# Performance work log

Hardware: AMD Instinct MI355X
Metric: run time of the kernel (lower is better)

Reference implementation:

```python
import jax, jax.numpy as jnp
from jax import lax
import numpy as np

IN_C = 256
PREV_IN_C = 256
OUT_C = 128
ATTN = IN_C // 8  # attn_size == attn_out == 32


def setup_inputs() -> dict:
    key = jax.random.key(0)
    ks = jax.random.split(key, 12)
    B, W, H = 4, 64, 64
    s = 0.02
    return {
        "source_enc_f": jax.random.normal(ks[0], (B, IN_C, W, H), jnp.float32),
        "target_enc_f": jax.random.normal(ks[1], (B, IN_C, W, H), jnp.float32),
        "prev_inp": jax.random.normal(ks[2], (B, PREV_IN_C, W // 2, H // 2), jnp.float32),
        "key_w": s * jax.random.normal(ks[3], (ATTN, IN_C), jnp.float32),
        "key_b": jnp.zeros((ATTN,), jnp.float32),
        "query_w": s * jax.random.normal(ks[4], (ATTN, IN_C), jnp.float32),
        "query_b": jnp.zeros((ATTN,), jnp.float32),
        "lin_w": s * jax.random.normal(ks[5], (ATTN, 2 * ATTN), jnp.float32),  # k_q_linear: cat([key, query])
        "lin_b": jnp.zeros((ATTN,), jnp.float32),
        "attn_w": s * jax.random.normal(ks[6], (IN_C, ATTN + IN_C), jnp.float32),
        "attn_b": jnp.zeros((IN_C,), jnp.float32),
        "gamma": jnp.array(0.1, jnp.float32),  # torch inits 0.0; nonzero so attn path is exercised
        "conv_w": s * jax.random.normal(ks[7], (OUT_C, IN_C + PREV_IN_C, 3, 3), jnp.float32),
        "conv_b": jnp.zeros((OUT_C,), jnp.float32),
    }


def _forward(source_enc_f, target_enc_f, prev_inp, key_w, key_b, query_w, query_b,
             lin_w, lin_b, attn_w, attn_b, gamma, conv_w, conv_b):
    B, C, W, H = source_enc_f.shape
    WH = W * H
    A = ATTN
    # 1x1 convs for query/key
    q = jnp.einsum('oc,bchw->bohw', query_w, source_enc_f) + query_b[:, None, None]
    k = jnp.einsum('oc,bchw->bohw', key_w, target_enc_f) + key_b[:, None, None]
    # Original: for every (key pos a, query pos c) pair, Linear(cat(key[a], query[c])),
    # then sum over c. Linear is separable: out[a] = WH*(Wk@key[a] + b) + Wq @ sum_c query[c].
    Wk, Wq = lin_w[:, :A], lin_w[:, A:]
    key_term = jnp.einsum('oa,bahw->bohw', Wk, k)          # [B, attn_out, W, H]
    q_sum = jnp.einsum('oa,ba->bo', Wq, q.sum(axis=(2, 3)))  # [B, attn_out]
    attn_map = WH * (key_term + lin_b[:, None, None]) + q_sum[:, :, None, None]
    # attn_conv (1x1) over cat([target, attn_map])
    x = jnp.concatenate([target_enc_f, attn_map], axis=1)
    out = jnp.einsum('oc,bchw->bohw', attn_w, x) + attn_b[:, None, None]
    x = target_enc_f + gamma * out
    prev_up = jnp.repeat(jnp.repeat(prev_inp, 2, axis=2), 2, axis=3)
    x = jnp.concatenate([x, prev_up], axis=1)
    y = lax.conv_general_dilated(x, conv_w, (1, 1), 'SAME',
                                 dimension_numbers=('NCHW', 'OIHW', 'NCHW'))
    y = y + conv_b[:, None, None]
    mean = y.mean(axis=(2, 3), keepdims=True)
    var = y.var(axis=(2, 3), keepdims=True)  # biased, as torch InstanceNorm2d
    y = (y - mean) * lax.rsqrt(var + 1e-5)
    return jax.nn.relu(y)


def reference(source_enc_f, target_enc_f, prev_inp, key_w, key_b, query_w, query_b,
              lin_w, lin_b, attn_w, attn_b, gamma, conv_w, conv_b):
    return _forward(source_enc_f, target_enc_f, prev_inp, key_w, key_b, query_w, query_b,
                    lin_w, lin_b, attn_w, attn_b, gamma, conv_w, conv_b)
```

## Files before the change

### kernel.cpp

```cpp
#include <hip/hip_runtime.h>

typedef unsigned short u16;
typedef __attribute__((ext_vector_type(8))) __bf16 bf16x8;
typedef __attribute__((ext_vector_type(8))) unsigned short u16x8;
typedef __attribute__((ext_vector_type(4))) float f32x4;

__device__ __forceinline__ u16 f2bf(float f) {
  unsigned u = __builtin_bit_cast(unsigned, f);
  unsigned r = u + 0x7fffu + ((u >> 16) & 1u);
  return (u16)(r >> 16);
}

__device__ __forceinline__ float wave_sum(float v) {
#pragma unroll
  for (int o = 32; o; o >>= 1) v += __shfl_xor(v, o, 64);
  return v;
}

__device__ __forceinline__ void gl2lds16(const u16* g, u16* l) {
  __builtin_amdgcn_global_load_lds(
      (const __attribute__((address_space(1))) unsigned int*)(const void*)g,
      (__attribute__((address_space(3))) unsigned int*)(void*)l, 16, 0, 0);
}

__global__ void k_pre(const float* __restrict__ tgt, const float* __restrict__ prev,
                      const float* __restrict__ src, const float* __restrict__ kw,
                      const float* __restrict__ lw, const float* __restrict__ aw,
                      const float* __restrict__ gamma,
                      u16* __restrict__ xin, float* __restrict__ ssum,
                      float* __restrict__ Mt) {
  __shared__ u16 lt[16896];
  int tid = threadIdx.x;
  if (blockIdx.x >= 1280) {
    float* E = (float*)lt;
    int o = blockIdx.x - 1280;
    if (tid < 32) {
      float s = 0.f;
      for (int o2 = 0; o2 < 32; ++o2) s += aw[o * 288 + 256 + o2] * lw[o2 * 64 + tid];
      E[tid] = s;
    }
    __syncthreads();
    float s = 0.f;
    for (int a = 0; a < 32; ++a) s += E[a] * kw[a * 256 + tid];
    Mt[o * 256 + tid] = gamma[0] * (aw[o * 288 + tid] + 4096.f * s) + (o == tid ? 1.f : 0.f);
    return;
  }
  if (blockIdx.x >= 256) {
    float* red = (float*)lt;
    int plane = blockIdx.x - 256;
    const float* p = src + (size_t)plane * 4096;
    float s = 0.f;
#pragma unroll
    for (int i = 0; i < 4; ++i) {
      f32x4 v = *(const f32x4*)(p + (i * 256 + tid) * 4);
      s += v[0] + v[1] + v[2] + v[3];
    }
    s = wave_sum(s);
    if ((tid & 63) == 0) red[tid >> 6] = s;
    __syncthreads();
    if (tid == 0) ssum[plane] = red[0] + red[1] + red[2] + red[3];
    return;
  }
  int b = blockIdx.x >> 6, h = blockIdx.x & 63;
  u16* slab = xin + (size_t)(b * 64 + h) * 40960;
  for (int i = tid; i < 8192; i += 256) {
    int cg = i >> 9, rest = i & 511;
    int colidx = rest >> 5, e = rest & 31;
    int pxp = (colidx == 0) ? 0 : (64 + colidx);
    slab[cg * 2560 + pxp * 32 + e] = 0;
  }
  for (int it = 0; it < 16; ++it) {
    int fi = it * 256 + tid;
    int c = fi >> 4, w4 = fi & 15;
    f32x4 v = *(const f32x4*)(tgt + ((size_t)(b * 256 + c) * 64 + h) * 64 + w4 * 4);
    int base = c * 66 + w4 * 4;
    lt[base] = f2bf(v[0]); lt[base + 1] = f2bf(v[1]);
    lt[base + 2] = f2bf(v[2]); lt[base + 3] = f2bf(v[3]);
  }
  __syncthreads();
  for (int it = 0; it < 8; ++it) {
    int i = it * 256 + tid;
    int o = i & 31, w = i >> 5;
    u16x8 v;
#pragma unroll
    for (int k = 0; k < 8; ++k) v[k] = lt[(o * 8 + k) * 66 + w];
    int cg = o >> 2, g = o & 3, pxp = w + 1;
    int slot = g ^ ((pxp >> 1) & 3);
    *(u16x8*)(slab + cg * 2560 + pxp * 32 + slot * 8) = v;
  }
  __syncthreads();
  for (int it = 0; it < 8; ++it) {
    int pi = it * 256 + tid;
    int cc = pi >> 3, wq = pi & 7;
    f32x4 v = *(const f32x4*)(prev + ((size_t)(b * 256 + cc) * 32 + (h >> 1)) * 32 + wq * 4);
    int base = cc * 66 + wq * 8;
    u16 b0 = f2bf(v[0]), b1 = f2bf(v[1]), b2 = f2bf(v[2]), b3 = f2bf(v[3]);
    lt[base] = b0; lt[base + 1] = b0; lt[base + 2] = b1; lt[base + 3] = b1;
    lt[base + 4] = b2; lt[base + 5] = b2; lt[base + 6] = b3; lt[base + 7] = b3;
  }
  __syncthreads();
  for (int it = 0; it < 8; ++it) {
    int i = it * 256 + tid;
    int o = i & 31, w = i >> 5;
    u16x8 v;
#pragma unroll
    for (int k = 0; k < 8; ++k) v[k] = lt[(o * 8 + k) * 66 + w];
    int cg = 8 + (o >> 2), g = o & 3, pxp = w + 1;
    int slot = g ^ ((pxp >> 1) & 3);
    *(u16x8*)(slab + cg * 2560 + pxp * 32 + slot * 8) = v;
  }
}

__global__ void k_w3(const float* __restrict__ cw, const float* __restrict__ Mt,
                     const float* __restrict__ ssum,
                     const float* __restrict__ qw, const float* __restrict__ qb,
                     const float* __restrict__ kb, const float* __restrict__ lw,
                     const float* __restrict__ lb, const float* __restrict__ aw,
                     const float* __restrict__ ab, const float* __restrict__ gamma,
                     u16* __restrict__ w3, float* __restrict__ cd2) {
  __shared__ float qs_l[128], amap_l[128], dvec_l[1024];
  __shared__ float cwl[4096];
  __shared__ float part[512];
  int tid = threadIdx.x;
  if (tid < 128) {
    int bb = tid >> 5, o = tid & 31;
    float s = 4096.f * qb[o];
    for (int c = 0; c < 256; ++c) s += qw[o * 256 + c] * ssum[bb * 256 + c];
    qs_l[tid] = s;
  }
  __syncthreads();
  if (tid < 128) {
    int bb = tid >> 5, o2 = tid & 31;
    float s = 0.f, kt = 0.f;
    for (int o = 0; o < 32; ++o) {
      s += lw[o2 * 64 + 32 + o] * qs_l[bb * 32 + o];
      kt += lw[o2 * 64 + o] * kb[o];
    }
    amap_l[tid] = 4096.f * (kt + lb[o2]) + s;
  }
  __syncthreads();
  float g = gamma[0];
  for (int i = tid; i < 1024; i += 512) {
    int bb = i >> 8, c = i & 255;
    float s = ab[c];
    for (int o2 = 0; o2 < 32; ++o2) s += aw[c * 288 + 256 + o2] * amap_l[bb * 32 + o2];
    dvec_l[i] = g * s;
  }
  int blk = blockIdx.x;
  int tap = blk >> 4, ocg = blk & 15;
  for (int e = tid; e < 4096; e += 512) {
    int oc = e >> 9, c = e & 511;
    cwl[e] = cw[(size_t)((ocg * 8 + oc) * 512 + c) * 9 + tap];
  }
  __syncthreads();
  int wv = tid >> 6, l = tid & 63;
  int c2 = l * 4;
  f32x4 acc = {0.f, 0.f, 0.f, 0.f};
  for (int c = 0; c < 256; ++c) {
    float wc = cwl[wv * 512 + c];
    f32x4 m = *(const f32x4*)(Mt + c * 256 + c2);
#pragma unroll
    for (int j = 0; j < 4; ++j) acc[j] += wc * m[j];
  }
  int ocf = ocg * 8 + wv;
#pragma unroll
  for (int j2 = 0; j2 < 4; ++j2) {
    int cf = c2 + j2;
    w3[(tap * 16 + (cf >> 5)) * 4096 + ((cf >> 3) & 3) * 1024 + ocf * 8 + (cf & 7)] = f2bf(acc[j2]);
    cf = 256 + c2 + j2;
    w3[(tap * 16 + (cf >> 5)) * 4096 + ((cf >> 3) & 3) * 1024 + ocf * 8 + (cf & 7)] =
        f2bf(cwl[wv * 512 + (c2 + j2 + 256)]);
  }
  {
    int bb = tid >> 7, oc = (tid >> 4) & 7, cp = tid & 15;
    float s = 0.f;
#pragma unroll
    for (int i = 0; i < 16; ++i) s += cwl[oc * 512 + cp * 16 + i] * dvec_l[bb * 256 + cp * 16 + i];
    part[tid] = s;
  }
  __syncthreads();
  if (tid < 32) {
    int bb = tid >> 3, oc = tid & 7;
    float s = 0.f;
#pragma unroll
    for (int cp = 0; cp < 16; ++cp) s += part[bb * 128 + oc * 16 + cp];
    cd2[(size_t)(bb * 128 + ocg * 8 + oc) * 9 + tap] = s;
  }
}

__global__ __launch_bounds__(512) void k_conv(const u16* __restrict__ xin,
                                              const u16* __restrict__ w3,
                                              const float* __restrict__ cd2,
                                              float* __restrict__ out) {
  __shared__ u16 lds[52736];
  const int XIN0 = 36864, DUMMY = 52224;
  int bid = blockIdx.x;
  int lid = (bid & 7) * 32 + (bid >> 3);
  int b = lid >> 6, h = lid & 63;
  int tid = threadIdx.x, l = tid & 63, wv = tid >> 6;
  int wr = wv & 3, wpx = wv >> 2;
  int r = l & 15, kb4 = l >> 4;

  if (h == 0 || h == 63) {
    int row = (h == 0) ? 0 : 2;
    for (int i = tid; i < 640; i += 512) {
      int bu = i / 320, off = (i % 320) * 8;
      u16x8 zz;
#pragma unroll
      for (int q = 0; q < 8; ++q) zz[q] = 0;
      *(u16x8*)(lds + XIN0 + bu * 7680 + row * 2560 + off) = zz;
    }
  }

  auto ISSUE_W3 = [&](int c2, int dy2, int buf, bool dummy) {
    u16* dst0 = lds + buf * 12288;
#pragma unroll
    for (int i = 0; i < 3; ++i) {
      int k = wv + 8 * i;
      int dx = k >> 3, part = k & 7;
      const u16* src = dummy ? (w3 + l * 8)
          : (w3 + (size_t)(((dy2 * 3 + dx) * 16 + c2) << 12) + part * 512 + l * 8);
      u16* dst = dummy ? (lds + DUMMY) : (dst0 + dx * 4096 + part * 512);
      gl2lds16(src, dst);
    }
  };
  auto ISSUE_XIN = [&](int c1, int buf, bool dummyAll) {
    u16* dst0 = lds + XIN0 + buf * 7680;
#pragma unroll
    for (int i = 0; i < 2; ++i) {
      int k = wv + 8 * i;
      int row = k / 5, part = k - row * 5;
      int grow = h - 1 + row;
      bool dm = dummyAll || (k == 15) || ((unsigned)grow >= 64u);
      const u16* src = dm ? (xin + l * 8)
          : (xin + ((size_t)(b * 64 + grow) * 16 + c1) * 2560 + part * 512 + l * 8);
      u16* dst = dm ? (lds + DUMMY) : (dst0 + row * 2560 + part * 512);
      gl2lds16(src, dst);
    }
  };

  f32x4 acc[2][2];
#pragma unroll
  for (int mf = 0; mf < 2; ++mf)
#pragma unroll
    for (int nf = 0; nf < 2; ++nf) acc[mf][nf] = f32x4{0.f, 0.f, 0.f, 0.f};

  ISSUE_W3(0, 0, 0, false);
  ISSUE_XIN(0, 0, false);
  ISSUE_W3(0, 1, 1, false);

  for (int c = 0; c < 16; ++c) {
#pragma unroll
    for (int dy = 0; dy < 3; ++dy) {
      if (dy == 0) asm volatile("s_waitcnt vmcnt(3) lgkmcnt(0)" ::: "memory");
      else         asm volatile("s_waitcnt vmcnt(5) lgkmcnt(0)" ::: "memory");
      __builtin_amdgcn_s_barrier();
      __builtin_amdgcn_sched_barrier(0);
      {
        int c2 = c + ((dy + 2) / 3);
        ISSUE_W3(c2, (dy + 2) % 3, (dy + 2) % 3, c2 > 15);
      }
      if (dy == 0) ISSUE_XIN(c + 1, (c + 1) & 1, c + 1 > 15);
      const u16* wbuf = lds + dy * 12288;
      const u16* xrow = lds + XIN0 + (c & 1) * 7680 + dy * 2560;
#pragma unroll
      for (int dx = 0; dx < 3; ++dx) {
        bf16x8 av[2];
#pragma unroll
        for (int mf = 0; mf < 2; ++mf)
          av[mf] = *(const bf16x8*)(wbuf + dx * 4096 + kb4 * 1024 + (wr * 32 + mf * 16 + r) * 8);
        bf16x8 bv[2];
#pragma unroll
        for (int nf = 0; nf < 2; ++nf) {
          int pxp = wpx * 32 + nf * 16 + r + dx;
          int slot = kb4 ^ ((pxp >> 1) & 3);
          bv[nf] = *(const bf16x8*)(xrow + pxp * 32 + slot * 8);
        }
#pragma unroll
        for (int mf = 0; mf < 2; ++mf)
#pragma unroll
          for (int nf = 0; nf < 2; ++nf)
            acc[mf][nf] = __builtin_amdgcn_mfma_f32_16x16x32_bf16(av[mf], bv[nf], acc[mf][nf], 0, 0, 0);
      }
    }
  }

  bool dy0v = (h > 0), dy2v = (h < 63);
#pragma unroll
  for (int mf = 0; mf < 2; ++mf) {
#pragma unroll
    for (int j = 0; j < 4; ++j) {
      int oc = wr * 32 + mf * 16 + kb4 * 4 + j;
      const float* cd = cd2 + (size_t)(b * 128 + oc) * 9;
      float sAll = 0.f, sL = 0.f, sR = 0.f;
#pragma unroll
      for (int dy3 = 0; dy3 < 3; ++dy3) {
        bool v = (dy3 == 1) || (dy3 == 0 ? dy0v : dy2v);
        if (v) {
          sAll += cd[dy3 * 3] + cd[dy3 * 3 + 1] + cd[dy3 * 3 + 2];
          sL += cd[dy3 * 3];
          sR += cd[dy3 * 3 + 2];
        }
      }
#pragma unroll
      for (int nf = 0; nf < 2; ++nf) {
        int px = wpx * 32 + nf * 16 + r;
        float corr = sAll - (px == 0 ? sL : 0.f) - (px == 63 ? sR : 0.f);
        out[(size_t)(b * 128 + oc) * 4096 + h * 64 + px] = acc[mf][nf][j] + corr;
      }
    }
  }
}

__global__ void k_norm(float* __restrict__ out) {
  int plane = blockIdx.x;
  float* p = out + (size_t)plane * 4096;
  int t = threadIdx.x;
  f32x4 v[4];
  float s = 0.f, s2 = 0.f;
#pragma unroll
  for (int i = 0; i < 4; ++i) {
    v[i] = *(const f32x4*)(p + (i * 256 + t) * 4);
#pragma unroll
    for (int k = 0; k < 4; ++k) { s += v[i][k]; s2 += v[i][k] * v[i][k]; }
  }
  s = wave_sum(s); s2 = wave_sum(s2);
  __shared__ float rs[4], rs2[4];
  if ((t & 63) == 0) { rs[t >> 6] = s; rs2[t >> 6] = s2; }
  __syncthreads();
  float S = rs[0] + rs[1] + rs[2] + rs[3];
  float S2 = rs2[0] + rs2[1] + rs2[2] + rs2[3];
  float mean = S * (1.f / 4096.f);
  float var = S2 * (1.f / 4096.f) - mean * mean;
  float inv = rsqrtf(var + 1e-5f);
#pragma unroll
  for (int i = 0; i < 4; ++i) {
    f32x4 o;
#pragma unroll
    for (int k = 0; k < 4; ++k) {
      float y = (v[i][k] - mean) * inv;
      o[k] = y > 0.f ? y : 0.f;
    }
    *(f32x4*)(p + (i * 256 + t) * 4) = o;
  }
}

extern "C" void kernel_launch(void* const* d_in, const int* in_sizes, int n_in,
                              void* d_out, int out_size, void* d_ws, size_t ws_size,
                              hipStream_t stream) {
  const float* src    = (const float*)d_in[0];
  const float* tgt    = (const float*)d_in[1];
  const float* prev   = (const float*)d_in[2];
  const float* key_w  = (const float*)d_in[3];
  const float* key_b  = (const float*)d_in[4];
  const float* qry_w  = (const float*)d_in[5];
  const float* qry_b  = (const float*)d_in[6];
  const float* lin_w  = (const float*)d_in[7];
  const float* lin_b  = (const float*)d_in[8];
  const float* attn_w = (const float*)d_in[9];
  const float* attn_b = (const float*)d_in[10];
  const float* gamma  = (const float*)d_in[11];
  const float* conv_w = (const float*)d_in[12];

  char* ws = (char*)d_ws;
  size_t off = 0;
  u16*   xin  = (u16*)(ws + off);  off += 20971520;
  float* ssum = (float*)(ws + off); off += 4096;
  float* Mt   = (float*)(ws + off); off += 262144;
  float* cd2  = (float*)(ws + off); off += 18432;
  u16*   w3   = (u16*)(ws + off);  off += 1179648;
  float* out  = (float*)d_out;

  k_pre<<<1536, 256, 0, stream>>>(tgt, prev, src, key_w, lin_w, attn_w, gamma,
                                  xin, ssum, Mt);
  k_w3<<<144, 512, 0, stream>>>(conv_w, Mt, ssum, qry_w, qry_b, key_b, lin_w, lin_b,
                                attn_w, attn_b, gamma, w3, cd2);
  k_conv<<<256, 512, 0, stream>>>(xin, w3, cd2, out);
  k_norm<<<512, 256, 0, stream>>>(out);
}
```

Measured before the change: 74.62 us.

## Regroup preprocessing kernels so xin packing overlaps weight folding

The preprocessing work is split differently across launches. The first kernel now does only the source plane sums and the Mt matrix. The second kernel runs the bf16 packing of target and prev into xin alongside the w3/cd2 weight folding, which only depend on the first kernel. Packing blocks go from 256 to 512 threads and use vectorized 16-byte zero stores for the padding. The aim is to hide the small, latency-bound weight-folding blocks behind the bandwidth-heavy packing, at the cost of a larger, mixed-role kernel whose LDS footprint may limit occupancy.

```diff
diff --git a/kernel.cpp b/kernel.cpp
--- a/kernel.cpp
+++ b/kernel.cpp
@@ -23,54 +23,136 @@
       (__attribute__((address_space(3))) unsigned int*)(void*)l, 16, 0, 0);
 }
 
-__global__ void k_pre(const float* __restrict__ tgt, const float* __restrict__ prev,
-                      const float* __restrict__ src, const float* __restrict__ kw,
-                      const float* __restrict__ lw, const float* __restrict__ aw,
-                      const float* __restrict__ gamma,
-                      u16* __restrict__ xin, float* __restrict__ ssum,
-                      float* __restrict__ Mt) {
-  __shared__ u16 lt[16896];
+__global__ void k0(const float* __restrict__ src, const float* __restrict__ kw,
+                   const float* __restrict__ lw, const float* __restrict__ aw,
+                   const float* __restrict__ gamma,
+                   float* __restrict__ ssum, float* __restrict__ Mt) {
+  __shared__ float red[64];
   int tid = threadIdx.x;
-  if (blockIdx.x >= 1280) {
-    float* E = (float*)lt;
-    int o = blockIdx.x - 1280;
+  if (blockIdx.x >= 1024) {
+    int o = blockIdx.x - 1024;
     if (tid < 32) {
       float s = 0.f;
       for (int o2 = 0; o2 < 32; ++o2) s += aw[o * 288 + 256 + o2] * lw[o2 * 64 + tid];
-      E[tid] = s;
+      red[tid] = s;
     }
     __syncthreads();
     float s = 0.f;
-    for (int a = 0; a < 32; ++a) s += E[a] * kw[a * 256 + tid];
+    for (int a = 0; a < 32; ++a) s += red[a] * kw[a * 256 + tid];
     Mt[o * 256 + tid] = gamma[0] * (aw[o * 288 + tid] + 4096.f * s) + (o == tid ? 1.f : 0.f);
     return;
   }
+  int plane = blockIdx.x;
+  const float* p = src + (size_t)plane * 4096;
+  float s = 0.f;
+#pragma unroll
+  for (int i = 0; i < 4; ++i) {
+    f32x4 v = *(const f32x4*)(p + (i * 256 + tid) * 4);
+    s += v[0] + v[1] + v[2] + v[3];
+  }
+  s = wave_sum(s);
+  if ((tid & 63) == 0) red[tid >> 6] = s;
+  __syncthreads();
+  if (tid == 0) ssum[plane] = red[0] + red[1] + red[2] + red[3];
+}
+
+__global__ void k1(const float* __restrict__ tgt, const float* __restrict__ prev,
+                   const float* __restrict__ cw, const float* __restrict__ Mt,
+                   const float* __restrict__ ssum,
+                   const float* __restrict__ qw, const float* __restrict__ qb,
+                   const float* __restrict__ kb, const float* __restrict__ lw,
+                   const float* __restrict__ lb, const float* __restrict__ aw,
+                   const float* __restrict__ ab, const float* __restrict__ gamma,
+                   u16* __restrict__ xin, u16* __restrict__ w3,
+                   float* __restrict__ cd2) {
+  int tid = threadIdx.x;
   if (blockIdx.x >= 256) {
-    float* red = (float*)lt;
-    int plane = blockIdx.x - 256;
-    const float* p = src + (size_t)plane * 4096;
-    float s = 0.f;
-#pragma unroll
-    for (int i = 0; i < 4; ++i) {
-      f32x4 v = *(const f32x4*)(p + (i * 256 + tid) * 4);
-      s += v[0] + v[1] + v[2] + v[3];
-    }
-    s = wave_sum(s);
-    if ((tid & 63) == 0) red[tid >> 6] = s;
-    __syncthreads();
-    if (tid == 0) ssum[plane] = red[0] + red[1] + red[2] + red[3];
+    __shared__ float qs_l[128], amap_l[128], dvec_l[1024];
+    __shared__ float cwl[4096];
+    __shared__ float part[512];
+    if (tid < 128) {
+      int bb = tid >> 5, o = tid & 31;
+      float s = 4096.f * qb[o];
+      for (int c = 0; c < 256; ++c) s += qw[o * 256 + c] * ssum[bb * 256 + c];
+      qs_l[tid] = s;
+    }
+    __syncthreads();
+    if (tid < 128) {
+      int bb = tid >> 5, o2 = tid & 31;
+      float s = 0.f, kt = 0.f;
+      for (int o = 0; o < 32; ++o) {
+        s += lw[o2 * 64 + 32 + o] * qs_l[bb * 32 + o];
+        kt += lw[o2 * 64 + o] * kb[o];
+      }
+      amap_l[tid] = 4096.f * (kt + lb[o2]) + s;
+    }
+    __syncthreads();
+    float g = gamma[0];
+    for (int i = tid; i < 1024; i += 512) {
+      int bb = i >> 8, c = i & 255;
+      float s = ab[c];
+      for (int o2 = 0; o2 < 32; ++o2) s += aw[c * 288 + 256 + o2] * amap_l[bb * 32 + o2];
+      dvec_l[i] = g * s;
+    }
+    int blk = blockIdx.x - 256;
+    int tap = blk >> 4, ocg = blk & 15;
+    for (int e = tid; e < 4096; e += 512) {
+      int oc = e >> 9, c = e & 511;
+      cwl[e] = cw[(size_t)((ocg * 8 + oc) * 512 + c) * 9 + tap];
+    }
+    __syncthreads();
+    int wv = tid >> 6, l = tid & 63;
+    int c2 = l * 4;
+    f32x4 acc = {0.f, 0.f, 0.f, 0.f};
+    for (int c = 0; c < 256; ++c) {
+      float wc = cwl[wv * 512 + c];
+      f32x4 m = *(const f32x4*)(Mt + c * 256 + c2);
+#pragma unroll
+      for (int j = 0; j < 4; ++j) acc[j] += wc * m[j];
+    }
+    int ocf = ocg * 8 + wv;
+#pragma unroll
+    for (int j2 = 0; j2 < 4; ++j2) {
+      int cf = c2 + j2;
+      w3[(tap * 16 + (cf >> 5)) * 4096 + ((cf >> 3) & 3) * 1024 + ocf * 8 + (cf & 7)] = f2bf(acc[j2]);
+      cf = 256 + c2 + j2;
+      w3[(tap * 16 + (cf >> 5)) * 4096 + ((cf >> 3) & 3) * 1024 + ocf * 8 + (cf & 7)] =
+          f2bf(cwl[wv * 512 + (c2 + j2 + 256)]);
+    }
+    {
+      int bb = tid >> 7, oc = (tid >> 4) & 7, cp = tid & 15;
+      float s = 0.f;
+#pragma unroll
+      for (int i = 0; i < 16; ++i) s += cwl[oc * 512 + cp * 16 + i] * dvec_l[bb * 256 + cp * 16 + i];
+      part[tid] = s;
+    }
+    __syncthreads();
+    if (tid < 32) {
+      int bb = tid >> 3, oc = tid & 7;
+      float s = 0.f;
+#pragma unroll
+      for (int cp = 0; cp < 16; ++cp) s += part[bb * 128 + oc * 16 + cp];
+      cd2[(size_t)(bb * 128 + ocg * 8 + oc) * 9 + tap] = s;
+    }
     return;
   }
+  __shared__ u16 lt[16896];
   int b = blockIdx.x >> 6, h = blockIdx.x & 63;
   u16* slab = xin + (size_t)(b * 64 + h) * 40960;
-  for (int i = tid; i < 8192; i += 256) {
-    int cg = i >> 9, rest = i & 511;
-    int colidx = rest >> 5, e = rest & 31;
+#pragma unroll
+  for (int it = 0; it < 2; ++it) {
+    int i = it * 512 + tid;
+    int cg = i >> 6, rest = i & 63;
+    int colidx = rest >> 2, e8 = rest & 3;
     int pxp = (colidx == 0) ? 0 : (64 + colidx);
-    slab[cg * 2560 + pxp * 32 + e] = 0;
-  }
-  for (int it = 0; it < 16; ++it) {
-    int fi = it * 256 + tid;
+    u16x8 zz;
+#pragma unroll
+    for (int q = 0; q < 8; ++q) zz[q] = 0;
+    *(u16x8*)(slab + cg * 2560 + pxp * 32 + e8 * 8) = zz;
+  }
+#pragma unroll
+  for (int it = 0; it < 8; ++it) {
+    int fi = it * 512 + tid;
     int c = fi >> 4, w4 = fi & 15;
     f32x4 v = *(const f32x4*)(tgt + ((size_t)(b * 256 + c) * 64 + h) * 64 + w4 * 4);
     int base = c * 66 + w4 * 4;
@@ -78,9 +160,9 @@
     lt[base + 2] = f2bf(v[2]); lt[base + 3] = f2bf(v[3]);
   }
   __syncthreads();
-  for (int it = 0; it < 8; ++it) {
-    int i = it * 256 + tid;
-    int o = i & 31, w = i >> 5;
+#pragma unroll
+  for (int it = 0; it < 4; ++it) {
+    int o = it * 8 + (tid >> 6), w = tid & 63;
     u16x8 v;
 #pragma unroll
     for (int k = 0; k < 8; ++k) v[k] = lt[(o * 8 + k) * 66 + w];
@@ -89,8 +171,9 @@
     *(u16x8*)(slab + cg * 2560 + pxp * 32 + slot * 8) = v;
   }
   __syncthreads();
-  for (int it = 0; it < 8; ++it) {
-    int pi = it * 256 + tid;
+#pragma unroll
+  for (int it = 0; it < 4; ++it) {
+    int pi = it * 512 + tid;
     int cc = pi >> 3, wq = pi & 7;
     f32x4 v = *(const f32x4*)(prev + ((size_t)(b * 256 + cc) * 32 + (h >> 1)) * 32 + wq * 4);
     int base = cc * 66 + wq * 8;
@@ -99,92 +182,15 @@
     lt[base + 4] = b2; lt[base + 5] = b2; lt[base + 6] = b3; lt[base + 7] = b3;
   }
   __syncthreads();
-  for (int it = 0; it < 8; ++it) {
-    int i = it * 256 + tid;
-    int o = i & 31, w = i >> 5;
+#pragma unroll
+  for (int it = 0; it < 4; ++it) {
+    int o = it * 8 + (tid >> 6), w = tid & 63;
     u16x8 v;
 #pragma unroll
     for (int k = 0; k < 8; ++k) v[k] = lt[(o * 8 + k) * 66 + w];
     int cg = 8 + (o >> 2), g = o & 3, pxp = w + 1;
     int slot = g ^ ((pxp >> 1) & 3);
     *(u16x8*)(slab + cg * 2560 + pxp * 32 + slot * 8) = v;
-  }
-}
-
-__global__ void k_w3(const float* __restrict__ cw, const float* __restrict__ Mt,
-                     const float* __restrict__ ssum,
-                     const float* __restrict__ qw, const float* __restrict__ qb,
-                     const float* __restrict__ kb, const float* __restrict__ lw,
-                     const float* __restrict__ lb, const float* __restrict__ aw,
-                     const float* __restrict__ ab, const float* __restrict__ gamma,
-                     u16* __restrict__ w3, float* __restrict__ cd2) {
-  __shared__ float qs_l[128], amap_l[128], dvec_l[1024];
-  __shared__ float cwl[4096];
-  __shared__ float part[512];
-  int tid = threadIdx.x;
-  if (tid < 128) {
-    int bb = tid >> 5, o = tid & 31;
-    float s = 4096.f * qb[o];
-    for (int c = 0; c < 256; ++c) s += qw[o * 256 + c] * ssum[bb * 256 + c];
-    qs_l[tid] = s;
-  }
-  __syncthreads();
-  if (tid < 128) {
-    int bb = tid >> 5, o2 = tid & 31;
-    float s = 0.f, kt = 0.f;
-    for (int o = 0; o < 32; ++o) {
-      s += lw[o2 * 64 + 32 + o] * qs_l[bb * 32 + o];
-      kt += lw[o2 * 64 + o] * kb[o];
-    }
-    amap_l[tid] = 4096.f * (kt + lb[o2]) + s;
-  }
-  __syncthreads();
-  float g = gamma[0];
-  for (int i = tid; i < 1024; i += 512) {
-    int bb = i >> 8, c = i & 255;
-    float s = ab[c];
-    for (int o2 = 0; o2 < 32; ++o2) s += aw[c * 288 + 256 + o2] * amap_l[bb * 32 + o2];
-    dvec_l[i] = g * s;
-  }
-  int blk = blockIdx.x;
-  int tap = blk >> 4, ocg = blk & 15;
-  for (int e = tid; e < 4096; e += 512) {
-    int oc = e >> 9, c = e & 511;
-    cwl[e] = cw[(size_t)((ocg * 8 + oc) * 512 + c) * 9 + tap];
-  }
-  __syncthreads();
-  int wv = tid >> 6, l = tid & 63;
-  int c2 = l * 4;
-  f32x4 acc = {0.f, 0.f, 0.f, 0.f};
-  for (int c = 0; c < 256; ++c) {
-    float wc = cwl[wv * 512 + c];
-    f32x4 m = *(const f32x4*)(Mt + c * 256 + c2);
-#pragma unroll
-    for (int j = 0; j < 4; ++j) acc[j] += wc * m[j];
-  }
-  int ocf = ocg * 8 + wv;
-#pragma unroll
-  for (int j2 = 0; j2 < 4; ++j2) {
-    int cf = c2 + j2;
-    w3[(tap * 16 + (cf >> 5)) * 4096 + ((cf >> 3) & 3) * 1024 + ocf * 8 + (cf & 7)] = f2bf(acc[j2]);
-    cf = 256 + c2 + j2;
-    w3[(tap * 16 + (cf >> 5)) * 4096 + ((cf >> 3) & 3) * 1024 + ocf * 8 + (cf & 7)] =
-        f2bf(cwl[wv * 512 + (c2 + j2 + 256)]);
-  }
-  {
-    int bb = tid >> 7, oc = (tid >> 4) & 7, cp = tid & 15;
-    float s = 0.f;
-#pragma unroll
-    for (int i = 0; i < 16; ++i) s += cwl[oc * 512 + cp * 16 + i] * dvec_l[bb * 256 + cp * 16 + i];
-    part[tid] = s;
-  }
-  __syncthreads();
-  if (tid < 32) {
-    int bb = tid >> 3, oc = tid & 7;
-    float s = 0.f;
-#pragma unroll
-    for (int cp = 0; cp < 16; ++cp) s += part[bb * 128 + oc * 16 + cp];
-    cd2[(size_t)(bb * 128 + ocg * 8 + oc) * 9 + tap] = s;
   }
 }
 
@@ -371,10 +377,9 @@
   u16*   w3   = (u16*)(ws + off);  off += 1179648;
   float* out  = (float*)d_out;
 
-  k_pre<<<1536, 256, 0, stream>>>(tgt, prev, src, key_w, lin_w, attn_w, gamma,
-                                  xin, ssum, Mt);
-  k_w3<<<144, 512, 0, stream>>>(conv_w, Mt, ssum, qry_w, qry_b, key_b, lin_w, lin_b,
-                                attn_w, attn_b, gamma, w3, cd2);
+  k0<<<1280, 256, 0, stream>>>(src, key_w, lin_w, attn_w, gamma, ssum, Mt);
+  k1<<<400, 512, 0, stream>>>(tgt, prev, conv_w, Mt, ssum, qry_w, qry_b, key_b,
+                              lin_w, lin_b, attn_w, attn_b, gamma, xin, w3, cd2);
   k_conv<<<256, 512, 0, stream>>>(xin, w3, cd2, out);
   k_norm<<<512, 256, 0, stream>>>(out);
 }
```

Result: no change. 73.71 us (-1.2%).
